# Performance work log

Measured on AMD Instinct MI355X. Metric: run time of the kernel, lower is better.

## Reference

```python
import math
import jax, jax.numpy as jnp
import numpy as np
from jax.scipy.special import erf, erfinv, logsumexp

M = 250000          # number of (u, v) datapoints
P = 4               # n_phases
N_MC = 64           # MC samples per interface pair
IA, IB = np.triu_indices(P, 1)   # interface pair indices (Ia < Ib since I is increasing)
K = len(IA)                      # n_interfaces = 6
LOG2 = math.log(2.0)
LOG2PI = math.log(2.0 * math.pi)
LOG_GAMMA_3_2 = math.log(math.gamma(1.5))


def _logsinh(x):
    # numerically stable log(sinh(x)); x > 0 in all uses here
    s = jnp.abs(x)
    return -LOG2 + s + jnp.log1p(-jnp.exp(-2.0 * s))


def _log_bessel_05(x):
    # I_{1/2}(x) = sqrt(2/(pi x)) sinh(x)
    return 0.5 * LOG2 - 0.5 * jnp.log(math.pi * x) + _logsinh(x)


def setup_inputs() -> dict:
    key = jax.random.key(0)
    k0, k1, k2 = jax.random.split(key, 3)
    u = jax.random.uniform(k0, (M,), dtype=jnp.float32)                 # intensities in [0,1]
    v = jax.random.uniform(k1, (M,), dtype=jnp.float32) * 0.3 + 0.01    # gradient magnitudes > 0
    eps = jax.random.uniform(k2, (K, N_MC), dtype=jnp.float32)          # fresh MC draw per interface
    I = jnp.linspace(0.0, 1.0, P, dtype=jnp.float32)
    W = jnp.zeros((K + P,), dtype=jnp.float32)
    sigma_b = jnp.array([2.0], dtype=jnp.float32)
    sigma_n = jnp.array([0.1], dtype=jnp.float32)
    d = jnp.array([2.0], dtype=jnp.float32)
    r = jnp.array([0.05], dtype=jnp.float32)
    return {"u": u, "v": v, "eps": eps, "I": I, "W": W,
            "sigma_b": sigma_b, "sigma_n": sigma_n, "d": d, "r": r}


def reference(u, v, eps, I, W, sigma_b, sigma_n, d, r):
    sb = sigma_b[0]
    sn = sigma_n[0]
    dd = d[0]
    rho = jnp.tanh(r[0])
    sr = sn * jnp.sqrt(1.0 - rho)          # sigma_n * sqrt(1 - rho)
    s2 = sn ** 2 * (1.0 - rho)
    N = eps.shape[1]
    log_w = jax.nn.log_softmax(W)

    # interior phases: [P, M]
    interior = (LOG2 + 2.0 * jnp.log(v) - LOG_GAMMA_3_2 - 3.0 * jnp.log(sr)
                - (v / sr) ** 2 - jnp.log(sn) - 0.5 * LOG2PI
                - 0.5 * ((u - I[:, None]) / sn) ** 2)

    rows = [interior]
    log_v = jnp.log(v)
    v2 = v ** 2
    for k in range(K):  # small fixed loop over interface pairs
        Ia = I[IA[k]]
        Ib = I[IB[k]]
        x = eps[k] * 2.0 * dd * sb - dd * sb                              # [N]
        In = (erf(x / (math.sqrt(2.0) * sb)) + 1.0) * 0.5 * (Ib - Ia) + Ia  # [N]
        # log p(u | I): [N, M]
        lu = -jnp.log(sn) - 0.5 * LOG2PI - 0.5 * ((u[None, :] - In[:, None]) / sn) ** 2
        # G(I): [N]
        Gk = (Ib - Ia) / jnp.sqrt(2.0 * math.pi * sb ** 2) * jnp.exp(
            -erfinv(2.0 * (In - Ia) / (Ib - Ia) - 1.0) ** 2)
        # log p(v | I): [N, M]
        lb = _log_bessel_05(2.0 * v[None, :] * Gk[:, None] / s2)
        lv = (LOG2 - 2.0 * jnp.log(sr) + 1.5 * log_v[None, :]
              - 0.5 * jnp.log(Gk)[:, None] + lb
              - (v2[None, :] + Gk[:, None] ** 2) / s2)
        rows.append((-math.log(N) + logsumexp(lu + lv, axis=0))[None, :])

    log_p = jnp.concatenate(rows, axis=0)                 # [P + K, M]
    log_p_uv = logsumexp(log_w[:, None] + log_p, axis=0)  # [M]
    return -jnp.sum(log_p_uv) / u.shape[0]
```

## Files before the change

kernel.cpp:

```cpp
#include <hip/hip_runtime.h>
#include <math.h>

#define KN 384
#define TPB 256

__device__ double g_part[1024];
__device__ int    g_ctr = 0;

__device__ __forceinline__ float fexp2(float x) {
  return __builtin_amdgcn_exp2f(x);
}

__global__ __launch_bounds__(TPB, 4) void fused_kernel(
    const float* __restrict__ u, const float* __restrict__ v,
    const float* __restrict__ eps, const float* __restrict__ I,
    const float* __restrict__ W, const float* __restrict__ sb_,
    const float* __restrict__ sn_, const float* __restrict__ d_,
    const float* __restrict__ r_, float* __restrict__ out,
    int M, int nb) {
  __shared__ float stx[KN], sty[KN], stz[KN];
  __shared__ double red[TPB];
  __shared__ int    slast;
  const int tid = threadIdx.x;
  const int i   = blockIdx.x * TPB + tid;

  float uu = 0.f, vv = 1.f;
  if (i < M) { uu = u[i]; vv = v[i]; }

  const float sb  = sb_[0];
  const float sn  = sn_[0];
  const float dd  = d_[0];
  const float rho = tanhf(r_[0]);
  const float s2  = sn * sn * (1.f - rho);
  const float sr  = sqrtf(s2);
  const float isn = 1.f / sn;
  const float inv_s2 = 1.f / s2;
  const float LOG2E = 1.4426950408889634f;
  const float SQH   = sqrtf(0.5f * LOG2E);

  float wmax = W[0];
  for (int j = 1; j < 10; ++j) wmax = fmaxf(wmax, W[j]);
  float se = 0.f;
  for (int j = 0; j < 10; ++j) se += expf(W[j] - wmax);
  const float lse = wmax + logf(se);

  const float LOG2PI_ = 1.8378770664093453f;
  const float LOG2_   = 0.6931471805599453f;
  const float LGG32   = -0.12078223763524522f;
  const float LOGPI_  = 1.1447298858494002f;
  const float Cterm = -logf(sn) - 0.5f * LOG2PI_ - logf(sr) - 0.5f * LOGPI_;
  const float Cint0 = LOG2_ - LGG32 - 3.f * logf(sr) - logf(sn) - 0.5f * LOG2PI_;

  float wint[4], cq[4];
#pragma unroll
  for (int p = 0; p < 4; ++p) {
    wint[p] = expf(W[p] - lse + Cint0);
    cq[p]   = I[p] * isn * SQH;
  }

  const int IAc[6] = {0, 0, 0, 1, 1, 2};
  const int IBc[6] = {1, 2, 3, 2, 3, 3};
  for (int t = tid; t < KN; t += TPB) {
    const int k = t >> 6;
    const float Ia = I[IAc[k]], Ib = I[IBc[k]];
    const float wk = expf(W[4 + k] - lse + Cterm) * (1.0f / 64.0f);
    const float e  = eps[t];
    const float x  = e * 2.f * dd * sb - dd * sb;
    const float y  = x / (1.4142135623730951f * sb);
    const float In = (erff(y) + 1.f) * 0.5f * (Ib - Ia) + Ia;
    const float qq = 2.f * (In - Ia) / (Ib - Ia) - 1.f;
    const float gi = erfinvf(qq);
    const float G  = (Ib - Ia) * 0.3989422804014327f / sb * expf(-gi * gi);
    stx[t] = In * isn * SQH;
    sty[t] = 2.f * inv_s2 * G * LOG2E;
    stz[t] = wk * expf(-G * G * inv_s2) / G;
  }

  const float us = uu * isn * SQH;
  const float gg = fexp2(-vv * vv * inv_s2 * LOG2E);
  float aint = 0.f;
#pragma unroll
  for (int p = 0; p < 4; ++p) {
    const float dq = us - cq[p];
    aint = fmaf(wint[p], fexp2(-dq * dq), aint);
  }
  const float c0 = (i < M) ? vv * gg : 0.f;
  const float c1 = (i < M) ? vv * vv * gg * aint : 1.f;

  __syncthreads();

#define ENT(TX, TY, TZ, S)                         \
  {                                                \
    const float du = us - (TX);                    \
    const float nd = du * -du;                     \
    const float a1 = fmaf(vv, (TY), nd);           \
    const float a2 = fmaf(vv, -(TY), nd);          \
    S = fmaf((TZ), fexp2(a1), S);                  \
    S = fmaf(-(TZ), fexp2(a2), S);                 \
  }

  float S0 = 0.f, S1 = 0.f, S2 = 0.f, S3 = 0.f;
  float S4 = 0.f, S5 = 0.f, S6 = 0.f, S7 = 0.f;
  const float4* px = (const float4*)stx;
  const float4* py = (const float4*)sty;
  const float4* pz = (const float4*)stz;
  float4 Xa = px[0], Ya = py[0], Za = pz[0];
  float4 Xb = px[1], Yb = py[1], Zb = pz[1];
#pragma unroll 2
  for (int g = 1; g <= 48; ++g) {
    const int gn = (g < 48) ? g : 47;
    const float4 Xa2 = px[2 * gn + 0], Ya2 = py[2 * gn + 0], Za2 = pz[2 * gn + 0];
    const float4 Xb2 = px[2 * gn + 1], Yb2 = py[2 * gn + 1], Zb2 = pz[2 * gn + 1];
    ENT(Xa.x, Ya.x, Za.x, S0) ENT(Xa.y, Ya.y, Za.y, S1)
    ENT(Xa.z, Ya.z, Za.z, S2) ENT(Xa.w, Ya.w, Za.w, S3)
    ENT(Xb.x, Yb.x, Zb.x, S4) ENT(Xb.y, Yb.y, Zb.y, S5)
    ENT(Xb.z, Yb.z, Zb.z, S6) ENT(Xb.w, Yb.w, Zb.w, S7)
    Xa = Xa2; Ya = Ya2; Za = Za2;
    Xb = Xb2; Yb = Yb2; Zb = Zb2;
  }
#undef ENT
  const float S = ((S0 + S1) + (S2 + S3)) + ((S4 + S5) + (S6 + S7));

  double mysum = (double)__logf(fmaf(c0, S, c1));

  red[tid] = mysum;
  __syncthreads();
  for (int s = TPB / 2; s > 0; s >>= 1) {
    if (tid < s) red[tid] += red[tid + s];
    __syncthreads();
  }
  if (tid == 0)
    __hip_atomic_store(&g_part[blockIdx.x], red[0], __ATOMIC_RELAXED,
                       __HIP_MEMORY_SCOPE_AGENT);

  if (tid == 0) {
    const int c = __hip_atomic_fetch_add(&g_ctr, 1, __ATOMIC_ACQ_REL,
                                         __HIP_MEMORY_SCOPE_AGENT);
    slast = (c == nb - 1) ? 1 : 0;
  }
  __syncthreads();
  if (slast) {
    double s = 0.0;
    for (int j = tid; j < nb; j += TPB)
      s += __hip_atomic_load(&g_part[j], __ATOMIC_RELAXED,
                             __HIP_MEMORY_SCOPE_AGENT);
    red[tid] = s;
    __syncthreads();
    for (int k2 = TPB / 2; k2 > 0; k2 >>= 1) {
      if (tid < k2) red[tid] += red[tid + k2];
      __syncthreads();
    }
    if (tid == 0) {
      out[0] = (float)(-red[0] / (double)M);
      __hip_atomic_store(&g_ctr, 0, __ATOMIC_RELAXED,
                         __HIP_MEMORY_SCOPE_AGENT);
    }
  }
}

extern "C" void kernel_launch(void* const* d_in, const int* in_sizes, int n_in,
                              void* d_out, int out_size, void* d_ws, size_t ws_size,
                              hipStream_t stream) {
  const float* u   = (const float*)d_in[0];
  const float* v   = (const float*)d_in[1];
  const float* eps = (const float*)d_in[2];
  const float* I   = (const float*)d_in[3];
  const float* W   = (const float*)d_in[4];
  const float* sb  = (const float*)d_in[5];
  const float* sn  = (const float*)d_in[6];
  const float* dd  = (const float*)d_in[7];
  const float* r   = (const float*)d_in[8];
  const int M  = in_sizes[0];
  const int nb = (M + TPB - 1) / TPB;
  hipLaunchKernelGGL(fused_kernel, dim3(nb), dim3(TPB), 0, stream,
                     u, v, eps, I, W, sb, sn, dd, r, (float*)d_out, M, nb);
}
```

Baseline: 107.0 us.

## Split table precompute into prep kernel and read tables from global memory

Moves the per-sample interface table (erf/erfinv/exp per MC sample) and the header constants into a separate single-block prep kernel that writes them to device globals. The main kernel then reads these uniformly indexed values straight from global memory, likely as scalar loads, instead of having every block recompute them into LDS and synchronise. This removes redundant transcendental work across roughly 977 blocks and the LDS staging. In exchange it adds a second launch with a serial dependency, and the many scalar loads in the inner loop could add latency.

```diff
diff --git a/kernel.cpp b/kernel.cpp
--- a/kernel.cpp
+++ b/kernel.cpp
@@ -4,6 +4,8 @@
 #define KN 384
 #define TPB 256
 
+__device__ float  g_tx[KN], g_ty[KN], g_tz[KN];
+__device__ float  g_hdr[12];
 __device__ double g_part[1024];
 __device__ int    g_ctr = 0;
 
@@ -11,22 +13,12 @@
   return __builtin_amdgcn_exp2f(x);
 }
 
-__global__ __launch_bounds__(TPB, 4) void fused_kernel(
-    const float* __restrict__ u, const float* __restrict__ v,
+__global__ __launch_bounds__(KN) void prep_kernel(
     const float* __restrict__ eps, const float* __restrict__ I,
     const float* __restrict__ W, const float* __restrict__ sb_,
     const float* __restrict__ sn_, const float* __restrict__ d_,
-    const float* __restrict__ r_, float* __restrict__ out,
-    int M, int nb) {
-  __shared__ float stx[KN], sty[KN], stz[KN];
-  __shared__ double red[TPB];
-  __shared__ int    slast;
-  const int tid = threadIdx.x;
-  const int i   = blockIdx.x * TPB + tid;
-
-  float uu = 0.f, vv = 1.f;
-  if (i < M) { uu = u[i]; vv = v[i]; }
-
+    const float* __restrict__ r_) {
+  const int t = threadIdx.x;
   const float sb  = sb_[0];
   const float sn  = sn_[0];
   const float dd  = d_[0];
@@ -51,44 +43,59 @@
   const float Cterm = -logf(sn) - 0.5f * LOG2PI_ - logf(sr) - 0.5f * LOGPI_;
   const float Cint0 = LOG2_ - LGG32 - 3.f * logf(sr) - logf(sn) - 0.5f * LOG2PI_;
 
-  float wint[4], cq[4];
-#pragma unroll
-  for (int p = 0; p < 4; ++p) {
-    wint[p] = expf(W[p] - lse + Cint0);
-    cq[p]   = I[p] * isn * SQH;
+  if (t < 12) {
+    float h = 0.f;
+    if      (t == 0) h = isn * SQH;
+    else if (t == 1) h = inv_s2 * LOG2E;
+    else if (t < 6)  h = I[t - 2] * isn * SQH;
+    else if (t < 10) h = expf(W[t - 6] - lse + Cint0);
+    g_hdr[t] = h;
   }
 
   const int IAc[6] = {0, 0, 0, 1, 1, 2};
   const int IBc[6] = {1, 2, 3, 2, 3, 3};
-  for (int t = tid; t < KN; t += TPB) {
-    const int k = t >> 6;
-    const float Ia = I[IAc[k]], Ib = I[IBc[k]];
-    const float wk = expf(W[4 + k] - lse + Cterm) * (1.0f / 64.0f);
-    const float e  = eps[t];
-    const float x  = e * 2.f * dd * sb - dd * sb;
-    const float y  = x / (1.4142135623730951f * sb);
-    const float In = (erff(y) + 1.f) * 0.5f * (Ib - Ia) + Ia;
-    const float qq = 2.f * (In - Ia) / (Ib - Ia) - 1.f;
-    const float gi = erfinvf(qq);
-    const float G  = (Ib - Ia) * 0.3989422804014327f / sb * expf(-gi * gi);
-    stx[t] = In * isn * SQH;
-    sty[t] = 2.f * inv_s2 * G * LOG2E;
-    stz[t] = wk * expf(-G * G * inv_s2) / G;
-  }
+  const int k = t >> 6;
+  const float Ia = I[IAc[k]], Ib = I[IBc[k]];
+  const float wk = expf(W[4 + k] - lse + Cterm) * (1.0f / 64.0f);
+  const float e  = eps[t];
+  const float x  = e * 2.f * dd * sb - dd * sb;
+  const float y  = x / (1.4142135623730951f * sb);
+  const float In = (erff(y) + 1.f) * 0.5f * (Ib - Ia) + Ia;
+  const float qq = 2.f * (In - Ia) / (Ib - Ia) - 1.f;
+  const float gi = erfinvf(qq);
+  const float G  = (Ib - Ia) * 0.3989422804014327f / sb * expf(-gi * gi);
+  g_tx[t] = In * isn * SQH;
+  g_ty[t] = 2.f * inv_s2 * G * LOG2E;
+  g_tz[t] = wk * expf(-G * G * inv_s2) / G;
+}
 
-  const float us = uu * isn * SQH;
-  const float gg = fexp2(-vv * vv * inv_s2 * LOG2E);
+__global__ __launch_bounds__(TPB) void main_kernel(
+    const float* __restrict__ u, const float* __restrict__ v,
+    float* __restrict__ out, int M, int nb) {
+  __shared__ double red[TPB];
+  __shared__ int    slast;
+  const int tid = threadIdx.x;
+  const int i   = blockIdx.x * TPB + tid;
+
+  float uu = 0.f, vv = 1.f;
+  if (i < M) { uu = u[i]; vv = v[i]; }
+
+  const float husc = g_hdr[0];
+  const float hg   = g_hdr[1];
+
+  const float us = uu * husc;
+  const float gg = fexp2(-vv * vv * hg);
   float aint = 0.f;
 #pragma unroll
   for (int p = 0; p < 4; ++p) {
-    const float dq = us - cq[p];
-    aint = fmaf(wint[p], fexp2(-dq * dq), aint);
+    const float dq = us - g_hdr[2 + p];
+    aint = fmaf(g_hdr[6 + p], fexp2(-dq * dq), aint);
   }
   const float c0 = (i < M) ? vv * gg : 0.f;
   const float c1 = (i < M) ? vv * vv * gg * aint : 1.f;
 
-  __syncthreads();
-
+  float S0 = 0.f, S1 = 0.f, S2 = 0.f, S3 = 0.f;
+  float S4 = 0.f, S5 = 0.f, S6 = 0.f, S7 = 0.f;
 #define ENT(TX, TY, TZ, S)                         \
   {                                                \
     const float du = us - (TX);                    \
@@ -98,25 +105,19 @@
     S = fmaf((TZ), fexp2(a1), S);                  \
     S = fmaf(-(TZ), fexp2(a2), S);                 \
   }
-
-  float S0 = 0.f, S1 = 0.f, S2 = 0.f, S3 = 0.f;
-  float S4 = 0.f, S5 = 0.f, S6 = 0.f, S7 = 0.f;
-  const float4* px = (const float4*)stx;
-  const float4* py = (const float4*)sty;
-  const float4* pz = (const float4*)stz;
-  float4 Xa = px[0], Ya = py[0], Za = pz[0];
-  float4 Xb = px[1], Yb = py[1], Zb = pz[1];
-#pragma unroll 2
-  for (int g = 1; g <= 48; ++g) {
-    const int gn = (g < 48) ? g : 47;
-    const float4 Xa2 = px[2 * gn + 0], Ya2 = py[2 * gn + 0], Za2 = pz[2 * gn + 0];
-    const float4 Xb2 = px[2 * gn + 1], Yb2 = py[2 * gn + 1], Zb2 = pz[2 * gn + 1];
-    ENT(Xa.x, Ya.x, Za.x, S0) ENT(Xa.y, Ya.y, Za.y, S1)
-    ENT(Xa.z, Ya.z, Za.z, S2) ENT(Xa.w, Ya.w, Za.w, S3)
-    ENT(Xb.x, Yb.x, Zb.x, S4) ENT(Xb.y, Yb.y, Zb.y, S5)
-    ENT(Xb.z, Yb.z, Zb.z, S6) ENT(Xb.w, Yb.w, Zb.w, S7)
-    Xa = Xa2; Ya = Ya2; Za = Za2;
-    Xb = Xb2; Yb = Yb2; Zb = Zb2;
+  for (int g = 0; g < KN / 8; ++g) {
+    const int b = g * 8;
+    float X[8], Y[8], Z[8];
+#pragma unroll
+    for (int j = 0; j < 8; ++j) {
+      X[j] = g_tx[b + j];
+      Y[j] = g_ty[b + j];
+      Z[j] = g_tz[b + j];
+    }
+    ENT(X[0], Y[0], Z[0], S0) ENT(X[1], Y[1], Z[1], S1)
+    ENT(X[2], Y[2], Z[2], S2) ENT(X[3], Y[3], Z[3], S3)
+    ENT(X[4], Y[4], Z[4], S4) ENT(X[5], Y[5], Z[5], S5)
+    ENT(X[6], Y[6], Z[6], S6) ENT(X[7], Y[7], Z[7], S7)
   }
 #undef ENT
   const float S = ((S0 + S1) + (S2 + S3)) + ((S4 + S5) + (S6 + S7));
@@ -172,6 +173,9 @@
   const float* r   = (const float*)d_in[8];
   const int M  = in_sizes[0];
   const int nb = (M + TPB - 1) / TPB;
-  hipLaunchKernelGGL(fused_kernel, dim3(nb), dim3(TPB), 0, stream,
-                     u, v, eps, I, W, sb, sn, dd, r, (float*)d_out, M, nb);
+
+  hipLaunchKernelGGL(prep_kernel, dim3(1), dim3(KN), 0, stream,
+                     eps, I, W, sb, sn, dd, r);
+  hipLaunchKernelGGL(main_kernel, dim3(nb), dim3(TPB), 0, stream,
+                     u, v, (float*)d_out, M, nb);
 }
```

Result: no change. 106.9 us (-0.1%).
